# Kernel tuning notes

Measured on AMD Instinct MI355X. Metric: run time of the kernel, lower is better.

## Reference

```python
import jax, jax.numpy as jnp
import numpy as np


def setup_inputs() -> dict:
    key = jax.random.key(0)
    ks = jax.random.split(key, 5)
    B, N, C, H = 8, 8192, 512, 8
    scale = 1.0 / np.sqrt(C)
    return {
        "x": jax.random.normal(ks[0], (B, N, C), dtype=jnp.float32),
        "qk_w": jax.random.normal(ks[1], (2 * C, C), dtype=jnp.float32) * scale,
        "qk_b": jax.random.normal(ks[2], (2 * C,), dtype=jnp.float32) * 0.01,
        "lepe_w": jax.random.normal(ks[3], (C, 1, 3), dtype=jnp.float32) * 0.5,
        "lepe_b": jax.random.normal(ks[4], (C,), dtype=jnp.float32) * 0.01,
        "num_heads": H,
    }


def reference(x, qk_w, qk_b, lepe_w, lepe_b, num_heads):
    B, N, C = x.shape
    hd = C // num_heads
    # qk projection -> split into q, k; ELU(.)+1 feature map
    qk = x @ qk_w.T + qk_b                      # [B,N,2C]
    q = jax.nn.elu(qk[..., :C]) + 1.0
    k = jax.nn.elu(qk[..., C:]) + 1.0
    q = q.reshape(B, N, num_heads, hd).transpose(0, 2, 1, 3)  # [B,H,N,hd]
    k = k.reshape(B, N, num_heads, hd).transpose(0, 2, 1, 3)
    v = x.reshape(B, N, num_heads, hd).transpose(0, 2, 1, 3)
    # normalizer: z = 1 / (q . mean_n(k) + eps)
    k_mean = k.mean(axis=2)                                    # [B,H,hd]
    z = 1.0 / (jnp.einsum('bhnd,bhd->bhn', q, k_mean) + 1e-6)  # [B,H,N]
    # linear attention: kv = k^T v per head, then q @ kv
    kv = jnp.einsum('bhnd,bhne->bhde', k, v)                   # [B,H,hd,hd]
    attn = jnp.einsum('bhnd,bhde->bhne', q, kv) * z[..., None] # [B,H,N,hd]
    attn = attn.transpose(0, 2, 1, 3).reshape(B, N, C)
    # lepe: depthwise conv1d over tokens on v (== x after head reshape round-trip)
    vc = x.transpose(0, 2, 1)                                  # [B,C,N]
    lepe = jax.lax.conv_general_dilated(
        vc, lepe_w, window_strides=(1,), padding=((1, 1),),
        dimension_numbers=('NCH', 'OIH', 'NCH'), feature_group_count=C,
    ) + lepe_b[None, :, None]                                  # [B,C,N]
    return attn + lepe.transpose(0, 2, 1)
```

## Files before the change

kernel.cpp:

```cpp
#include <hip/hip_runtime.h>
#include <hip/hip_bf16.h>

#define B_    8
#define N_    8192
#define C_    512
#define H_    8
#define HD_   64
#define M_    (B_ * N_)
#define TWO_C 1024
#define LDA   40

typedef short short8 __attribute__((ext_vector_type(8)));
typedef float f32x4  __attribute__((ext_vector_type(4)));

__device__ __forceinline__ float bf2f(unsigned v) {
    return __uint_as_float(v << 16);
}

__device__ __forceinline__ unsigned f2bf(float f) {
    union { __hip_bfloat16 b; unsigned short u; } cv;
    cv.b = __float2bfloat16(f);
    return (unsigned)cv.u;
}

__device__ __forceinline__ uint2 pack4(float4 f) {
    uint2 r;
    r.x = f2bf(f.x) | (f2bf(f.y) << 16);
    r.y = f2bf(f.z) | (f2bf(f.w) << 16);
    return r;
}

__global__ __launch_bounds__(256) void conv_w_bf16(
    const float* __restrict__ w, unsigned short* __restrict__ wbf)
{
    const int i = (blockIdx.x * 256 + threadIdx.x) * 8;
    float4 a = *(const float4*)(w + i);
    float4 b = *(const float4*)(w + i + 4);
    uint2 pa = pack4(a), pb = pack4(b);
    *(uint4*)(wbf + i) = make_uint4(pa.x, pa.y, pb.x, pb.y);
}

__global__ __launch_bounds__(256, 2) void gemm_qk_mfma(
    const float* __restrict__ x, const unsigned short* __restrict__ wbf,
    const float* __restrict__ bias,
    __hip_bfloat16* __restrict__ qws, __hip_bfloat16* __restrict__ kws)
{
    __shared__ __align__(16) unsigned short As[128 * LDA];
    __shared__ __align__(16) unsigned short Bs[128 * LDA];

    const int t  = threadIdx.x;
    const int wv = t >> 6;
    const int ln = t & 63;

    const int L  = blockIdx.x;
    const int rp = (L & 7) + ((L >> 6) << 3);
    const int cp = (L >> 3) & 7;
    const int m0 = rp * 128;
    const int n0 = cp * 128;

    const int sr = t >> 2;
    const int sk = (t & 3) * 8;

    const int wm = wv & 1, wn = wv >> 1;
    const int fr = ln & 15;
    const int fk = (ln >> 4) * 8;

    f32x4 acc[4][4];
#pragma unroll
    for (int i = 0; i < 4; i++)
#pragma unroll
        for (int j = 0; j < 4; j++) acc[i][j] = {0.f, 0.f, 0.f, 0.f};

    const float* xa = x + (size_t)(m0 + sr) * C_ + sk;
    const unsigned short* wa = wbf + (size_t)(n0 + sr) * C_ + sk;

    for (int k0 = 0; k0 < C_; k0 += 32) {
        float4 a0 = *(const float4*)(xa + k0);
        float4 a1 = *(const float4*)(xa + k0 + 4);
        float4 a2 = *(const float4*)(xa + k0 + (size_t)64 * C_);
        float4 a3 = *(const float4*)(xa + k0 + (size_t)64 * C_ + 4);
        uint4  b0 = *(const uint4*)(wa + k0);
        uint4  b1 = *(const uint4*)(wa + k0 + (size_t)64 * C_);
        if (k0) __syncthreads();
        uint2 pa0 = pack4(a0), pa1 = pack4(a1), pa2 = pack4(a2), pa3 = pack4(a3);
        *(uint4*)&As[sr * LDA + sk]        = make_uint4(pa0.x, pa0.y, pa1.x, pa1.y);
        *(uint4*)&As[(sr + 64) * LDA + sk] = make_uint4(pa2.x, pa2.y, pa3.x, pa3.y);
        *(uint4*)&Bs[sr * LDA + sk]        = b0;
        *(uint4*)&Bs[(sr + 64) * LDA + sk] = b1;
        __syncthreads();

        short8 af[4], bfr[4];
#pragma unroll
        for (int i = 0; i < 4; i++)
            af[i] = *(const short8*)&As[(wm * 64 + i * 16 + fr) * LDA + fk];
#pragma unroll
        for (int j = 0; j < 4; j++)
            bfr[j] = *(const short8*)&Bs[(wn * 64 + j * 16 + fr) * LDA + fk];
#pragma unroll
        for (int i = 0; i < 4; i++)
#pragma unroll
            for (int j = 0; j < 4; j++)
                acc[i][j] = __builtin_amdgcn_mfma_f32_16x16x32_bf16(
                    af[i], bfr[j], acc[i][j], 0, 0, 0);
    }

    __hip_bfloat16* dst;
    int oc0;
    if (n0 < C_) { dst = qws; oc0 = n0; }
    else         { dst = kws; oc0 = n0 - C_; }
    float bv[4];
#pragma unroll
    for (int j = 0; j < 4; j++) bv[j] = bias[n0 + wn * 64 + j * 16 + fr];
    const int rb = (ln >> 4) * 4;
#pragma unroll
    for (int i = 0; i < 4; i++) {
#pragma unroll
        for (int r = 0; r < 4; r++) {
            const size_t m = (size_t)(m0 + wm * 64 + i * 16 + rb + r);
#pragma unroll
            for (int j = 0; j < 4; j++) {
                const int oc = oc0 + wn * 64 + j * 16 + fr;
                float v = acc[i][j][r] + bv[j];
                v = (v > 0.f) ? (v + 1.f) : __expf(v);
                dst[m * C_ + oc] = __float2bfloat16(v);
            }
        }
    }
}

__global__ __launch_bounds__(256) void kv_partial(
    const __hip_bfloat16* __restrict__ kws, const float* __restrict__ x,
    float* __restrict__ kvT, float* __restrict__ kmean)
{
    __shared__ float kt[32][64];
    __shared__ float vt[32][64];
    const int t  = threadIdx.x;
    const int s  = blockIdx.x;
    const int bh = blockIdx.y;
    const int b  = bh >> 3, h = bh & 7;
    const int td = t >> 4, te = t & 15;
    const int kr = t >> 3;
    const int kc = (t & 7) * 8;
    const int vr = t >> 4;
    const int vc = (t & 15) * 4;

    const size_t base = (size_t)b * N_ * C_ + h * HD_;

    float acc[4][4];
    float ksum[4] = {0.f, 0.f, 0.f, 0.f};
#pragma unroll
    for (int i = 0; i < 4; i++)
#pragma unroll
        for (int j = 0; j < 4; j++) acc[i][j] = 0.f;

    const int nstart = s * (N_ / 16);
    for (int n0 = nstart; n0 < nstart + N_ / 16; n0 += 32) {
        uint4  ku = *(const uint4*)&kws[base + (size_t)(n0 + kr) * C_ + kc];
        float4 v0 = *(const float4*)&x[base + (size_t)(n0 + vr) * C_ + vc];
        float4 v1 = *(const float4*)&x[base + (size_t)(n0 + vr + 16) * C_ + vc];
        __syncthreads();
        kt[kr][kc + 0] = bf2f(ku.x & 0xffffu); kt[kr][kc + 1] = bf2f(ku.x >> 16);
        kt[kr][kc + 2] = bf2f(ku.y & 0xffffu); kt[kr][kc + 3] = bf2f(ku.y >> 16);
        kt[kr][kc + 4] = bf2f(ku.z & 0xffffu); kt[kr][kc + 5] = bf2f(ku.z >> 16);
        kt[kr][kc + 6] = bf2f(ku.w & 0xffffu); kt[kr][kc + 7] = bf2f(ku.w >> 16);
        *(float4*)&vt[vr][vc]      = v0;
        *(float4*)&vt[vr + 16][vc] = v1;
        __syncthreads();
#pragma unroll
        for (int nn = 0; nn < 32; nn++) {
            float4 kd = *(const float4*)&kt[nn][td * 4];
            float4 ve = *(const float4*)&vt[nn][te * 4];
            float kr4[4] = {kd.x, kd.y, kd.z, kd.w};
            float vr4[4] = {ve.x, ve.y, ve.z, ve.w};
#pragma unroll
            for (int i = 0; i < 4; i++)
#pragma unroll
                for (int j = 0; j < 4; j++) acc[i][j] += kr4[i] * vr4[j];
            ksum[0] += kd.x; ksum[1] += kd.y; ksum[2] += kd.z; ksum[3] += kd.w;
        }
    }

    float* kvp = kvT + (size_t)bh * HD_ * HD_;
#pragma unroll
    for (int i = 0; i < 4; i++)
#pragma unroll
        for (int j = 0; j < 4; j++)
            atomicAdd(&kvp[(te * 4 + j) * HD_ + td * 4 + i], acc[i][j]);
    if (te == 0) {
#pragma unroll
        for (int i = 0; i < 4; i++)
            atomicAdd(&kmean[bh * HD_ + td * 4 + i], ksum[i] * (1.0f / N_));
    }
}

__global__ __launch_bounds__(256, 2) void out_mfma(
    const __hip_bfloat16* __restrict__ qws, const float* __restrict__ x,
    const float* __restrict__ kvT, const float* __restrict__ kmean,
    const float* __restrict__ lw, const float* __restrict__ lb,
    float* __restrict__ out)
{
    __shared__ __align__(16) unsigned short qs[128][72];
    __shared__ __align__(16) unsigned short kvs[64][72];
    __shared__ float xs[130][68];
    __shared__ float zz[128];
    __shared__ float pz[128][2];
    __shared__ float kms[64];
    __shared__ float lw0[64], lw1[64], lw2[64], lbs[64];

    const int t  = threadIdx.x;
    const int n0 = blockIdx.x * 128;
    const int bh = blockIdx.y;
    const int b  = bh >> 3, h = bh & 7;

    {
        const __hip_bfloat16* qp = qws + ((size_t)b * N_ + n0) * C_ + h * HD_;
        for (int i = t; i < 1024; i += 256) {
            const int r = i >> 3, c8 = (i & 7) * 8;
            uint4 u = *(const uint4*)&qp[(size_t)r * C_ + c8];
            *(uint4*)&qs[r][c8] = u;
        }
    }
    {
        const float* kvp = kvT + (size_t)bh * 4096;
        for (int i = t; i < 2048; i += 256) {
            const int e = i >> 5, d0 = (i & 31) * 2;
            float2 v = *(const float2*)&kvp[e * 64 + d0];
            *(unsigned*)&kvs[e][d0] = f2bf(v.x) | (f2bf(v.y) << 16);
        }
    }
    {
        for (int i = t; i < 130 * 16; i += 256) {
            const int r = i >> 4, c4 = (i & 15) * 4;
            const int n = n0 - 1 + r;
            float4 v = make_float4(0.f, 0.f, 0.f, 0.f);
            if (n >= 0 && n < N_)
                v = *(const float4*)&x[((size_t)b * N_ + n) * C_ + h * HD_ + c4];
            *(float4*)&xs[r][c4] = v;
        }
    }
    if (t < 64) {
        const int c = h * HD_ + t;
        lw0[t] = lw[c * 3 + 0];
        lw1[t] = lw[c * 3 + 1];
        lw2[t] = lw[c * 3 + 2];
        lbs[t] = lb[c];
        kms[t] = kmean[bh * HD_ + t];
    }
    __syncthreads();

    {
        const int nn = t >> 1, d0 = (t & 1) * 32;
        float s = 0.f;
        for (int d = d0; d < d0 + 32; d++) s += bf2f(qs[nn][d]) * kms[d];
        pz[nn][t & 1] = s;
    }
    __syncthreads();
    if (t < 128) zz[t] = 1.0f / (pz[t][0] + pz[t][1] + 1e-6f);
    __syncthreads();

    const int wv = t >> 6, ln = t & 63;
    const int fr = ln & 15;
    const int fk = (ln >> 4) * 8;
    const int r0 = wv * 32;

    f32x4 acc[2][4];
#pragma unroll
    for (int bd = 0; bd < 2; bd++)
#pragma unroll
        for (int c = 0; c < 4; c++) acc[bd][c] = {0.f, 0.f, 0.f, 0.f};

    short8 af[2][2], bfr[4][2];
#pragma unroll
    for (int bd = 0; bd < 2; bd++)
#pragma unroll
        for (int kk = 0; kk < 2; kk++)
            af[bd][kk] = *(const short8*)&qs[r0 + bd * 16 + fr][kk * 32 + fk];
#pragma unroll
    for (int c = 0; c < 4; c++)
#pragma unroll
        for (int kk = 0; kk < 2; kk++)
            bfr[c][kk] = *(const short8*)&kvs[c * 16 + fr][kk * 32 + fk];
#pragma unroll
    for (int bd = 0; bd < 2; bd++)
#pragma unroll
        for (int c = 0; c < 4; c++)
#pragma unroll
            for (int kk = 0; kk < 2; kk++)
                acc[bd][c] = __builtin_amdgcn_mfma_f32_16x16x32_bf16(
                    af[bd][kk], bfr[c][kk], acc[bd][c], 0, 0, 0);

    const int rb = (ln >> 4) * 4;
#pragma unroll
    for (int bd = 0; bd < 2; bd++) {
#pragma unroll
        for (int c = 0; c < 4; c++) {
            const int e = c * 16 + fr;
            const float w0 = lw0[e], w1 = lw1[e], w2 = lw2[e], bb = lbs[e];
#pragma unroll
            for (int r = 0; r < 4; r++) {
                const int nn = r0 + bd * 16 + rb + r;
                const float le = xs[nn][e] * w0 + xs[nn + 1][e] * w1
                               + xs[nn + 2][e] * w2 + bb;
                out[((size_t)b * N_ + n0 + nn) * C_ + h * HD_ + e] =
                    acc[bd][c][r] * zz[nn] + le;
            }
        }
    }
}

extern "C" void kernel_launch(void* const* d_in, const int* in_sizes, int n_in,
                              void* d_out, int out_size, void* d_ws, size_t ws_size,
                              hipStream_t stream)
{
    const float* x      = (const float*)d_in[0];
    const float* qk_w   = (const float*)d_in[1];
    const float* qk_b   = (const float*)d_in[2];
    const float* lepe_w = (const float*)d_in[3];
    const float* lepe_b = (const float*)d_in[4];
    float* out = (float*)d_out;

    char* ws = (char*)d_ws;
    __hip_bfloat16* qws = (__hip_bfloat16*)ws;
    __hip_bfloat16* kws = qws + (size_t)M_ * C_;
    float* kvT   = (float*)(ws + 2 * (size_t)M_ * C_ * sizeof(__hip_bfloat16));
    float* kmean = kvT + (size_t)64 * HD_ * HD_;
    unsigned short* wbf = (unsigned short*)kvT;

    conv_w_bf16<<<256, 256, 0, stream>>>(qk_w, wbf);
    gemm_qk_mfma<<<4096, 256, 0, stream>>>(x, wbf, qk_b, qws, kws);
    hipMemsetAsync(kvT, 0, (size_t)(64 * HD_ * HD_ + 64 * HD_) * sizeof(float),
                   stream);
    kv_partial<<<dim3(16, 64), 256, 0, stream>>>(kws, x, kvT, kmean);
    out_mfma<<<dim3(N_ / 128, B_ * H_), 256, 0, stream>>>(
        qws, x, kvT, kmean, lepe_w, lepe_b, out);
}
```

Measured before the change: 527.7 us.

## Pre-convert x to bf16 and use swizzled K=64 LDS tiles in QK GEMM

Adds a separate pass that converts x to bf16 into the output buffer, used as scratch, so the QK GEMM loads half-size bf16 operands instead of fp32 and skips in-loop packing. The GEMM K-step grows from 32 to 64 with an XOR-swizzled unpadded LDS layout, which avoids bank conflicts and halves the number of barriers. The cost is an extra full read of x (~128MB) plus a write of the bf16 copy (~64MB) in a separate kernel, and the GEMM still re-reads the bf16 x once per output-column tile.

Measured after the change: 717.9 us. 1.36x slower.

```diff
diff --git a/kernel.cpp b/kernel.cpp
--- a/kernel.cpp
+++ b/kernel.cpp
@@ -8,7 +8,6 @@
 #define HD_   64
 #define M_    (B_ * N_)
 #define TWO_C 1024
-#define LDA   40
 
 typedef short short8 __attribute__((ext_vector_type(8)));
 typedef float f32x4  __attribute__((ext_vector_type(4)));
@@ -40,13 +39,23 @@
     *(uint4*)(wbf + i) = make_uint4(pa.x, pa.y, pb.x, pb.y);
 }
 
+__global__ __launch_bounds__(256) void conv_x_bf16(
+    const float* __restrict__ x, unsigned short* __restrict__ xbf)
+{
+    const size_t i = ((size_t)blockIdx.x * 256 + threadIdx.x) * 8;
+    float4 a = *(const float4*)(x + i);
+    float4 b = *(const float4*)(x + i + 4);
+    uint2 pa = pack4(a), pb = pack4(b);
+    *(uint4*)(xbf + i) = make_uint4(pa.x, pa.y, pb.x, pb.y);
+}
+
 __global__ __launch_bounds__(256, 2) void gemm_qk_mfma(
-    const float* __restrict__ x, const unsigned short* __restrict__ wbf,
+    const unsigned short* __restrict__ xbf, const unsigned short* __restrict__ wbf,
     const float* __restrict__ bias,
     __hip_bfloat16* __restrict__ qws, __hip_bfloat16* __restrict__ kws)
 {
-    __shared__ __align__(16) unsigned short As[128 * LDA];
-    __shared__ __align__(16) unsigned short Bs[128 * LDA];
+    __shared__ __align__(16) unsigned short As[128 * 64];
+    __shared__ __align__(16) unsigned short Bs[128 * 64];
 
     const int t  = threadIdx.x;
     const int wv = t >> 6;
@@ -58,12 +67,9 @@
     const int m0 = rp * 128;
     const int n0 = cp * 128;
 
-    const int sr = t >> 2;
-    const int sk = (t & 3) * 8;
-
     const int wm = wv & 1, wn = wv >> 1;
     const int fr = ln & 15;
-    const int fk = (ln >> 4) * 8;
+    const int qg = ln >> 4;
 
     f32x4 acc[4][4];
 #pragma unroll
@@ -71,37 +77,56 @@
 #pragma unroll
         for (int j = 0; j < 4; j++) acc[i][j] = {0.f, 0.f, 0.f, 0.f};
 
-    const float* xa = x + (size_t)(m0 + sr) * C_ + sk;
-    const unsigned short* wa = wbf + (size_t)(n0 + sr) * C_ + sk;
-
-    for (int k0 = 0; k0 < C_; k0 += 32) {
-        float4 a0 = *(const float4*)(xa + k0);
-        float4 a1 = *(const float4*)(xa + k0 + 4);
-        float4 a2 = *(const float4*)(xa + k0 + (size_t)64 * C_);
-        float4 a3 = *(const float4*)(xa + k0 + (size_t)64 * C_ + 4);
-        uint4  b0 = *(const uint4*)(wa + k0);
-        uint4  b1 = *(const uint4*)(wa + k0 + (size_t)64 * C_);
+    const unsigned short* xa = xbf + (size_t)m0 * C_;
+    const unsigned short* wa = wbf + (size_t)n0 * C_;
+
+    for (int k0 = 0; k0 < C_; k0 += 64) {
+        uint4 av[4], bv4[4];
+#pragma unroll
+        for (int it = 0; it < 4; it++) {
+            const int g = it * 256 + t;
+            const int r = g >> 3, s = g & 7;
+            av[it]  = *(const uint4*)(xa + (size_t)r * C_ + k0 + s * 8);
+            bv4[it] = *(const uint4*)(wa + (size_t)r * C_ + k0 + s * 8);
+        }
         if (k0) __syncthreads();
-        uint2 pa0 = pack4(a0), pa1 = pack4(a1), pa2 = pack4(a2), pa3 = pack4(a3);
-        *(uint4*)&As[sr * LDA + sk]        = make_uint4(pa0.x, pa0.y, pa1.x, pa1.y);
-        *(uint4*)&As[(sr + 64) * LDA + sk] = make_uint4(pa2.x, pa2.y, pa3.x, pa3.y);
-        *(uint4*)&Bs[sr * LDA + sk]        = b0;
-        *(uint4*)&Bs[(sr + 64) * LDA + sk] = b1;
+#pragma unroll
+        for (int it = 0; it < 4; it++) {
+            const int g = it * 256 + t;
+            const int r = g >> 3, s = g & 7;
+            const int slot = s ^ (r & 7);
+            *(uint4*)&As[r * 64 + slot * 8] = av[it];
+            *(uint4*)&Bs[r * 64 + slot * 8] = bv4[it];
+        }
         __syncthreads();
 
-        short8 af[4], bfr[4];
+        short8 af[4][2], bfr[4][2];
+#pragma unroll
+        for (int i = 0; i < 4; i++) {
+            const int r = wm * 64 + i * 16 + fr;
+#pragma unroll
+            for (int kk = 0; kk < 2; kk++) {
+                const int slot = (kk * 4 + qg) ^ (fr & 7);
+                af[i][kk] = *(const short8*)&As[r * 64 + slot * 8];
+            }
+        }
+#pragma unroll
+        for (int j = 0; j < 4; j++) {
+            const int r = wn * 64 + j * 16 + fr;
+#pragma unroll
+            for (int kk = 0; kk < 2; kk++) {
+                const int slot = (kk * 4 + qg) ^ (fr & 7);
+                bfr[j][kk] = *(const short8*)&Bs[r * 64 + slot * 8];
+            }
+        }
 #pragma unroll
         for (int i = 0; i < 4; i++)
-            af[i] = *(const short8*)&As[(wm * 64 + i * 16 + fr) * LDA + fk];
-#pragma unroll
-        for (int j = 0; j < 4; j++)
-            bfr[j] = *(const short8*)&Bs[(wn * 64 + j * 16 + fr) * LDA + fk];
-#pragma unroll
-        for (int i = 0; i < 4; i++)
 #pragma unroll
             for (int j = 0; j < 4; j++)
-                acc[i][j] = __builtin_amdgcn_mfma_f32_16x16x32_bf16(
-                    af[i], bfr[j], acc[i][j], 0, 0, 0);
+#pragma unroll
+                for (int kk = 0; kk < 2; kk++)
+                    acc[i][j] = __builtin_amdgcn_mfma_f32_16x16x32_bf16(
+                        af[i][kk], bfr[j][kk], acc[i][j], 0, 0, 0);
     }
 
     __hip_bfloat16* dst;
@@ -325,9 +350,11 @@
     float* kvT   = (float*)(ws + 2 * (size_t)M_ * C_ * sizeof(__hip_bfloat16));
     float* kmean = kvT + (size_t)64 * HD_ * HD_;
     unsigned short* wbf = (unsigned short*)kvT;
+    unsigned short* xbf = (unsigned short*)d_out;
 
     conv_w_bf16<<<256, 256, 0, stream>>>(qk_w, wbf);
-    gemm_qk_mfma<<<4096, 256, 0, stream>>>(x, wbf, qk_b, qws, kws);
+    conv_x_bf16<<<M_ * C_ / (256 * 8), 256, 0, stream>>>(x, xbf);
+    gemm_qk_mfma<<<4096, 256, 0, stream>>>(xbf, wbf, qk_b, qws, kws);
     hipMemsetAsync(kvT, 0, (size_t)(64 * HD_ * HD_ + 64 * HD_) * sizeof(float),
                    stream);
     kv_partial<<<dim3(16, 64), 256, 0, stream>>>(kws, x, kvT, kmean);
```
